# Optimization experiments

Measured on AMD Instinct MI355X. Metric: run time of the kernel, lower is better.

## Reference

```python
import jax, jax.numpy as jnp
import numpy as np

LN_EPS = 1e-5


def _layernorm(x, gamma, beta):
    mu = jnp.mean(x, axis=-1, keepdims=True)
    var = jnp.mean(jnp.square(x - mu), axis=-1, keepdims=True)
    return (x - mu) / jnp.sqrt(var + LN_EPS) * gamma + beta


def setup_inputs() -> dict:
    key = jax.random.key(0)
    ks = jax.random.split(key, 4)
    B, T, H, L = 32, 2048, 512, 2
    scale = 1.0 / np.sqrt(H)  # matches torch GRU uniform(-1/sqrt(H),1/sqrt(H)) scale
    x = jax.random.normal(ks[0], (B, T, H), dtype=jnp.float32)
    W_ih = jax.random.normal(ks[1], (L, 3 * H, H), dtype=jnp.float32) * scale
    W_hh = jax.random.normal(ks[2], (L, 3 * H, H), dtype=jnp.float32) * scale
    b_ih = jnp.zeros((L, 3 * H), dtype=jnp.float32)
    b_hh = jnp.zeros((L, 3 * H), dtype=jnp.float32)
    gamma = jnp.ones((H,), dtype=jnp.float32)
    beta = jnp.zeros((H,), dtype=jnp.float32)
    return {"x": x, "gamma": gamma, "beta": beta,
            "W_ih": W_ih, "W_hh": W_hh, "b_ih": b_ih, "b_hh": b_hh}


def reference(x, gamma, beta, W_ih, W_hh, b_ih, b_hh):
    # LayerNorm then multi-layer GRU (PyTorch gate order: r, z, n).
    B, T, H = x.shape
    L = W_ih.shape[0]
    h = _layernorm(x, gamma, beta)
    for l in range(L):
        # Precompute input projections for all timesteps: [B, T, 3H]
        xp = jnp.einsum('bth,gh->btg', h, W_ih[l]) + b_ih[l]
        Whh_l = W_hh[l]
        bhh_l = b_hh[l]

        def step(h_prev, xp_t):
            hp = h_prev @ Whh_l.T + bhh_l              # [B, 3H]
            xr, xz, xn = jnp.split(xp_t, 3, axis=-1)
            hr, hz, hn = jnp.split(hp, 3, axis=-1)
            r = jax.nn.sigmoid(xr + hr)
            z = jax.nn.sigmoid(xz + hz)
            n = jnp.tanh(xn + r * hn)
            h_new = (1.0 - z) * n + z * h_prev
            return h_new, h_new

        h0 = jnp.zeros((B, H), dtype=x.dtype)
        _, ys = jax.lax.scan(step, h0, jnp.swapaxes(xp, 0, 1))  # [T, B, H]
        h = jnp.swapaxes(ys, 0, 1)
    return h
```

## Files before the change

kernel.cpp:

```cpp
#include <hip/hip_runtime.h>
#include <hip/hip_fp16.h>

typedef float f32x4 __attribute__((ext_vector_type(4)));
typedef float f32x16 __attribute__((ext_vector_type(16)));
typedef _Float16 half8 __attribute__((ext_vector_type(8)));
typedef _Float16 half2t __attribute__((ext_vector_type(2)));
typedef unsigned int u32;
typedef u32 u32x4v __attribute__((ext_vector_type(4)));

#define DEVI static __device__ __forceinline__

constexpr int BATCH = 32;
constexpr int TLEN  = 2048;
constexpr int HDIM  = 512;
constexpr int G3    = 1536;
constexpr u32 POIS  = 0xFFFFFFFFu;
constexpr int NSLOT = 16;

DEVI float fast_sigmoid(float x) { return 1.0f / (1.0f + __expf(-x)); }

DEVI float fast_tanh(float x) {
  const float ax = fabsf(x);
  const float t = __expf(-2.0f * ax);
  const float r = (1.0f - t) / (1.0f + t);
  return copysignf(r, x);
}

DEVI u32 pack2h(float a, float b) {
  return __builtin_bit_cast(u32, __builtin_amdgcn_cvt_pkrtz(a, b));
}

DEVI u32 llc_load32(const u32* p) {
  return __hip_atomic_load(p, __ATOMIC_RELAXED, __HIP_MEMORY_SCOPE_AGENT);
}
DEVI void llc_store32(u32* p, u32 v) {
  __hip_atomic_store(p, v, __ATOMIC_RELAXED, __HIP_MEMORY_SCOPE_AGENT);
}

DEVI u32x4v llc_load128_async(const u32* p) {
  u32x4v r;
  asm volatile("global_load_dwordx4 %0, %1, off sc0 sc1" : "=&v"(r) : "v"(p));
  return r;
}

DEVI int chk4(u32x4v v) {
  return (int)((v[0] == POIS) | (v[1] == POIS) | (v[2] == POIS) | (v[3] == POIS));
}

__global__ void convert_weights(const float* __restrict__ wih, const float* __restrict__ whh,
                                _Float16* __restrict__ wih_h, _Float16* __restrict__ whh_h)
{
  const size_t n = (size_t)2 * G3 * HDIM;
  for (size_t i = (size_t)blockIdx.x * blockDim.x + threadIdx.x; i < n;
       i += (size_t)gridDim.x * blockDim.x) {
    wih_h[i] = (_Float16)wih[i];
    whh_h[i] = (_Float16)whh[i];
  }
}

__global__ __launch_bounds__(256) void ln_kernel(const float* __restrict__ x,
    const float* __restrict__ gamma, const float* __restrict__ beta,
    _Float16* __restrict__ out)
{
  const int row = blockIdx.x;
  const int tid = threadIdx.x;
  const float* xr = x + (size_t)row * HDIM;
  float a = xr[tid], b = xr[tid + 256];
  float s = a + b, ss = a * a + b * b;
#pragma unroll
  for (int m = 1; m < 64; m <<= 1) {
    s  += __shfl_xor(s, m, 64);
    ss += __shfl_xor(ss, m, 64);
  }
  __shared__ float sb[8];
  const int w = tid >> 6;
  if ((tid & 63) == 0) { sb[w] = s; sb[4 + w] = ss; }
  __syncthreads();
  s  = sb[0] + sb[1] + sb[2] + sb[3];
  ss = sb[4] + sb[5] + sb[6] + sb[7];
  const float mu   = s * (1.0f / HDIM);
  const float var  = ss * (1.0f / HDIM) - mu * mu;
  const float rstd = rsqrtf(var + 1e-5f);
  out[(size_t)row * HDIM + tid]       = (_Float16)((a - mu) * rstd * gamma[tid] + beta[tid]);
  out[(size_t)row * HDIM + tid + 256] = (_Float16)((b - mu) * rstd * gamma[tid + 256] + beta[tid + 256]);
}

__global__ __launch_bounds__(256) void gemm_f16(
    const _Float16* __restrict__ A, const _Float16* __restrict__ W,
    const float* __restrict__ bias, _Float16* __restrict__ C,
    int t0, int lgT)
{
  __shared__ _Float16 As[128][40];
  __shared__ _Float16 Bs[128][40];
  const int bm = blockIdx.x;
  const int bn = blockIdx.y;
  const int tid = threadIdx.x;
  const int lane = tid & 63;
  const int wv = tid >> 6;
  const int wm = wv >> 1, wn = wv & 1;
  const int l15 = lane & 15, g4 = lane >> 4;
  const int tmask = (1 << lgT) - 1;

  f32x4 zero4 = {0.f, 0.f, 0.f, 0.f};
  f32x4 acc[4][4];
#pragma unroll
  for (int i = 0; i < 4; ++i) {
#pragma unroll
    for (int j = 0; j < 4; ++j) acc[i][j] = zero4;
  }

  const int srow = tid >> 2;
  const int scol = (tid & 3) * 8;
  size_t arow[2];
#pragma unroll
  for (int r2 = 0; r2 < 2; ++r2) {
    int m = bm * 128 + r2 * 64 + srow;
    int b = m >> lgT, tt = m & tmask;
    arow[r2] = ((size_t)b * TLEN + (size_t)(t0 + tt)) * HDIM;
  }
  const size_t brow0 = (size_t)(bn * 128 + srow) * HDIM;

  for (int kt = 0; kt < HDIM; kt += 32) {
#pragma unroll
    for (int r2 = 0; r2 < 2; ++r2) {
      *(uint4*)&As[r2 * 64 + srow][scol] = *(const uint4*)&A[arow[r2] + kt + scol];
      *(uint4*)&Bs[r2 * 64 + srow][scol] = *(const uint4*)&W[brow0 + (size_t)r2 * 64 * HDIM + kt + scol];
    }
    __syncthreads();
    half8 af[4], bf[4];
#pragma unroll
    for (int i = 0; i < 4; ++i) af[i] = *(const half8*)&As[wm * 64 + i * 16 + l15][g4 * 8];
#pragma unroll
    for (int j = 0; j < 4; ++j) bf[j] = *(const half8*)&Bs[wn * 64 + j * 16 + l15][g4 * 8];
#pragma unroll
    for (int i = 0; i < 4; ++i) {
#pragma unroll
      for (int j = 0; j < 4; ++j)
        acc[i][j] = __builtin_amdgcn_mfma_f32_16x16x32_f16(af[i], bf[j], acc[i][j], 0, 0, 0);
    }
    __syncthreads();
  }
#pragma unroll
  for (int j = 0; j < 4; ++j) {
    const int col = bn * 128 + wn * 64 + j * 16 + l15;
    const float bi = bias[col];
#pragma unroll
    for (int i = 0; i < 4; ++i) {
      const int mrow = bm * 128 + wm * 64 + i * 16 + g4 * 4;
#pragma unroll
      for (int r = 0; r < 4; ++r)
        C[(size_t)(mrow + r) * G3 + col] = (_Float16)(acc[i][j][r] + bi);
    }
  }
}

__global__ void init_sync(u32* __restrict__ h1ring, u32* __restrict__ h2ring,
                          u32* __restrict__ syncw)
{
  const int i = blockIdx.x * 256 + threadIdx.x;
  const u32 v = (i >> 13) == 0 ? 0u : POIS;
  h1ring[i] = v;
  h2ring[i] = v;
  if (i == 0) syncw[0] = 0u;
}

__global__ __launch_bounds__(512, 1) void gru_fused(
    const u32* __restrict__ xp,
    const u32* __restrict__ whh,
    const u32* __restrict__ wih2,
    const float* __restrict__ bhh,
    const float* __restrict__ bih2,
    float* __restrict__ out,
    u32* __restrict__ h1ring,
    u32* __restrict__ h2ring,
    u32* __restrict__ syncw,
    int t0, int t1, int lgT)
{
  const int l2 = blockIdx.x >> 4;
  const int c  = blockIdx.x & 15;
  const int tid = threadIdx.x;
  const int lane = tid & 63;
  const int w = tid >> 6;
  const int l31 = lane & 31;
  const int kh = lane >> 5;

  __shared__ __align__(16) u32 st_l[32 * 260];
  __shared__ __align__(16) u32 h1_l[32 * 260];
  __shared__ float sg_h[96 * 33];
  __shared__ float sg_i[96 * 33];

  half8 bf[32];
  const bool mfma_w = (w < 3) || (l2 && w < 6);
  if (mfma_w) {
    const int gt = (w < 3) ? w : w - 3;
    const int grow = gt * 512 + c * 32 + l31;
    const u32* wsrc = (w < 3) ? (whh + (size_t)l2 * (G3 * 256)) : wih2;
#pragma unroll
    for (int ks = 0; ks < 32; ++ks)
      bf[ks] = *(const half8*)&wsrc[(size_t)grow * 256 + ks * 8 + kh * 4];
  }

  const int dp = tid & 15;
  const int ga = tid >> 4;
  const float* bhh_l = bhh + l2 * G3;
  float biasH[3][2], biasI[3][2];
#pragma unroll
  for (int gt = 0; gt < 3; ++gt) {
    biasH[gt][0] = bhh_l[gt * 512 + c * 32 + 2 * dp];
    biasH[gt][1] = bhh_l[gt * 512 + c * 32 + 2 * dp + 1];
    biasI[gt][0] = l2 ? bih2[gt * 512 + c * 32 + 2 * dp] : 0.0f;
    biasI[gt][1] = l2 ? bih2[gt * 512 + c * 32 + 2 * dp + 1] : 0.0f;
  }

  u32* const ringOwn = l2 ? h2ring : h1ring;

  for (int t = t0; t < t1; ++t) {
    u32 xu[3];
    if (!l2) {
      const size_t row = ((size_t)(ga << lgT) + (size_t)(t - t0)) * 768;
#pragma unroll
      for (int gt = 0; gt < 3; ++gt)
        xu[gt] = xp[row + gt * 256 + c * 16 + dp];
    }

    const u32* rdA = ringOwn + (size_t)(t & 15) * 8192 + (tid << 2);
    const u32* rdB = h1ring + (size_t)((t + 1) & 15) * 8192 + (tid << 2);
    u32x4v a0, a1, a2, a3, b0, b1, b2, b3;
    while (true) {
      a0 = llc_load128_async(rdA);
      a1 = llc_load128_async(rdA + 2048);
      a2 = llc_load128_async(rdA + 4096);
      a3 = llc_load128_async(rdA + 6144);
      if (l2) {
        b0 = llc_load128_async(rdB);
        b1 = llc_load128_async(rdB + 2048);
        b2 = llc_load128_async(rdB + 4096);
        b3 = llc_load128_async(rdB + 6144);
      }
      u32 prog = 0;
      if (!l2) prog = llc_load32(&syncw[0]);
      asm volatile("s_waitcnt vmcnt(0)" ::: "memory");
      __builtin_amdgcn_sched_barrier(0);
      int bad = chk4(a0) | chk4(a1) | chk4(a2) | chk4(a3);
      if (l2) bad |= chk4(b0) | chk4(b1) | chk4(b2) | chk4(b3);
      else    bad |= (int)((int)prog < t - 3);
      if (!__any(bad)) break;
      __builtin_amdgcn_s_sleep(1);
    }
    {
      const int r0 = tid >> 6;
      const int cc = (tid << 2) & 255;
      *(u32x4v*)&st_l[(0  + r0) * 260 + cc] = a0;
      *(u32x4v*)&st_l[(8  + r0) * 260 + cc] = a1;
      *(u32x4v*)&st_l[(16 + r0) * 260 + cc] = a2;
      *(u32x4v*)&st_l[(24 + r0) * 260 + cc] = a3;
      if (l2) {
        *(u32x4v*)&h1_l[(0  + r0) * 260 + cc] = b0;
        *(u32x4v*)&h1_l[(8  + r0) * 260 + cc] = b1;
        *(u32x4v*)&h1_l[(16 + r0) * 260 + cc] = b2;
        *(u32x4v*)&h1_l[(24 + r0) * 260 + cc] = b3;
      }
    }
    __syncthreads();

    const u32 hpp = st_l[ga * 260 + c * 16 + dp];

    if (mfma_w) {
      f32x16 acc;
#pragma unroll
      for (int i = 0; i < 16; ++i) acc[i] = 0.0f;
      const u32* asrc = (w < 3) ? st_l : h1_l;
#pragma unroll
      for (int ks = 0; ks < 32; ++ks) {
        const half8 af = *(const half8*)&asrc[l31 * 260 + ks * 8 + kh * 4];
        acc = __builtin_amdgcn_mfma_f32_32x32x16_f16(af, bf[ks], acc, 0, 0, 0);
      }
      const int gt = (w < 3) ? w : w - 3;
      float* sg = (w < 3) ? sg_h : sg_i;
#pragma unroll
      for (int r = 0; r < 16; ++r) {
        const int grp = (r & 3) + 8 * (r >> 2) + 4 * kh;
        sg[(gt * 32 + l31) * 33 + grp] = acc[r];
      }
    }
    __syncthreads();

    float hn0, hn1;
    {
      const half2t hp2 = __builtin_bit_cast(half2t, hpp);
      float hn[2];
#pragma unroll
      for (int dd = 0; dd < 2; ++dd) {
        const int d = 2 * dp + dd;
        float xr, xz, xn;
        if (!l2) {
          const half2t xr2 = __builtin_bit_cast(half2t, xu[0]);
          const half2t xz2 = __builtin_bit_cast(half2t, xu[1]);
          const half2t xn2 = __builtin_bit_cast(half2t, xu[2]);
          xr = (float)(dd ? xr2.y : xr2.x);
          xz = (float)(dd ? xz2.y : xz2.x);
          xn = (float)(dd ? xn2.y : xn2.x);
        } else {
          xr = sg_i[(0 * 32 + d) * 33 + ga] + biasI[0][dd];
          xz = sg_i[(32 + d) * 33 + ga]     + biasI[1][dd];
          xn = sg_i[(64 + d) * 33 + ga]     + biasI[2][dd];
        }
        const float hprev = (float)(dd ? hp2.y : hp2.x);
        const float rr = fast_sigmoid(xr + sg_h[(0 * 32 + d) * 33 + ga] + biasH[0][dd]);
        const float zz = fast_sigmoid(xz + sg_h[(32 + d) * 33 + ga]     + biasH[1][dd]);
        const float nn = fast_tanh(xn + rr * (sg_h[(64 + d) * 33 + ga]  + biasH[2][dd]));
        hn[dd] = (1.0f - zz) * nn + zz * hprev;
      }
      hn0 = hn[0]; hn1 = hn[1];
    }
    const int my = ga * 256 + c * 16 + dp;
    llc_store32(&ringOwn[(size_t)((t + 1) & 15) * 8192 + my], pack2h(hn0, hn1));
    if (l2) {
      float2 v; v.x = hn0; v.y = hn1;
      *(float2*)&out[((size_t)ga * TLEN + t) * HDIM + c * 32 + 2 * dp] = v;
    }
    llc_store32(&ringOwn[(size_t)((t + 9) & 15) * 8192 + my], POIS);
    if (l2 && c == 0 && tid == 0) llc_store32(&syncw[0], (u32)(t + 1));
  }
}

extern "C" void kernel_launch(void* const* d_in, const int* in_sizes, int n_in,
                              void* d_out, int out_size, void* d_ws, size_t ws_size,
                              hipStream_t stream)
{
  const float* x     = (const float*)d_in[0];
  const float* gamma = (const float*)d_in[1];
  const float* beta  = (const float*)d_in[2];
  const float* Wih   = (const float*)d_in[3];
  const float* Whh   = (const float*)d_in[4];
  const float* bih   = (const float*)d_in[5];
  const float* bhh   = (const float*)d_in[6];
  float* out = (float*)d_out;

  const size_t wbytes  = (size_t)2 * G3 * HDIM * 2;
  const size_t hseqb   = (size_t)BATCH * TLEN * HDIM * 2;
  const size_t ringb   = (size_t)NSLOT * 8192 * 4;
  const size_t fixed   = hseqb + 2 * wbytes + 2 * ringb + 4096;
  int lgT = 11;
  while (lgT > 2 && ((size_t)BATCH * ((size_t)1 << lgT) * G3 * 2 + fixed) > ws_size) --lgT;
  const int TSEG = 1 << lgT;
  const int nseg = TLEN / TSEG;

  char* ws = (char*)d_ws;
  _Float16* xp     = (_Float16*)ws;
  char* base       = ws + (size_t)BATCH * TSEG * G3 * 2;
  _Float16* hseq   = (_Float16*)base;
  _Float16* wih_h  = (_Float16*)(base + hseqb);
  _Float16* whh_h  = (_Float16*)(base + hseqb + wbytes);
  u32*      h1ring = (u32*)    (base + hseqb + 2 * wbytes);
  u32*      h2ring = h1ring + (size_t)NSLOT * 8192;
  u32*      syncw  = h2ring + (size_t)NSLOT * 8192;

  convert_weights<<<512, 256, 0, stream>>>(Wih, Whh, wih_h, whh_h);
  ln_kernel<<<BATCH * TLEN, 256, 0, stream>>>(x, gamma, beta, hseq);
  init_sync<<<512, 256, 0, stream>>>(h1ring, h2ring, syncw);

  const dim3 ggrid(BATCH * TSEG / 128, 12);
  for (int s = 0; s < nseg; ++s) {
    const int t0 = s * TSEG;
    gemm_f16<<<ggrid, 256, 0, stream>>>(hseq, wih_h, bih, xp, t0, lgT);
    gru_fused<<<32, 512, 0, stream>>>((const u32*)xp, (const u32*)whh_h,
                                      (const u32*)(wih_h + (size_t)G3 * HDIM),
                                      bhh, bih + G3, out,
                                      h1ring, h2ring, syncw, t0, t0 + TSEG, lgT);
  }
}
```

Measured before the change: 8.701 ms.

## Restructure GRU recurrence MFMA into 16x16 tiles with in-register gate epilogue

The recurrent matmul moves from three 32x32x16 MFMA waves to four waves of 16x16x32 MFMA. Each wave computes all three gates for its own 16x16 tile, so the gate nonlinearity runs straight from accumulators and the sg_h LDS round trip and one barrier in layer 1 go away. The ring buffer layout changes to a per-block chunked fp16 layout written with 16-bit atomic stores, and the poison check now works per half. Each block's own previous h slice is read from LDS instead of polled from the ring. In exchange each writing thread issues more, smaller global stores, and a barrier is added at the end of every step.

```diff
diff --git a/kernel.cpp b/kernel.cpp
--- a/kernel.cpp
+++ b/kernel.cpp
@@ -6,6 +6,7 @@
 typedef _Float16 half8 __attribute__((ext_vector_type(8)));
 typedef _Float16 half2t __attribute__((ext_vector_type(2)));
 typedef unsigned int u32;
+typedef unsigned short u16;
 typedef u32 u32x4v __attribute__((ext_vector_type(4)));
 
 #define DEVI static __device__ __forceinline__
@@ -36,6 +37,9 @@
 DEVI void llc_store32(u32* p, u32 v) {
   __hip_atomic_store(p, v, __ATOMIC_RELAXED, __HIP_MEMORY_SCOPE_AGENT);
 }
+DEVI void llc_store16(u16* p, u16 v) {
+  __hip_atomic_store(p, v, __ATOMIC_RELAXED, __HIP_MEMORY_SCOPE_AGENT);
+}
 
 DEVI u32x4v llc_load128_async(const u32* p) {
   u32x4v r;
@@ -43,8 +47,14 @@
   return r;
 }
 
-DEVI int chk4(u32x4v v) {
-  return (int)((v[0] == POIS) | (v[1] == POIS) | (v[2] == POIS) | (v[3] == POIS));
+DEVI int chkH(u32x4v v) {
+  int b = 0;
+#pragma unroll
+  for (int i = 0; i < 4; ++i) {
+    const u32 x = v[i];
+    b |= (int)(((x & 0xFFFFu) == 0xFFFFu) | ((x >> 16) == 0xFFFFu));
+  }
+  return b;
 }
 
 __global__ void convert_weights(const float* __restrict__ wih, const float* __restrict__ whh,
@@ -181,48 +191,76 @@
   const int tid = threadIdx.x;
   const int lane = tid & 63;
   const int w = tid >> 6;
-  const int l31 = lane & 31;
-  const int kh = lane >> 5;
+  const int l15 = lane & 15;
+  const int g4 = (lane >> 4) & 3;
 
   __shared__ __align__(16) u32 st_l[32 * 260];
   __shared__ __align__(16) u32 h1_l[32 * 260];
-  __shared__ float sg_h[96 * 33];
   __shared__ float sg_i[96 * 33];
-
-  half8 bf[32];
-  const bool mfma_w = (w < 3) || (l2 && w < 6);
-  if (mfma_w) {
-    const int gt = (w < 3) ? w : w - 3;
+  __shared__ __align__(16) _Float16 own_h[1024];
+  u32* const own_hU = (u32*)own_h;
+
+  const bool isHH = (w < 4);
+  const bool isIH = l2 && (w >= 4) && (w < 7);
+  const int dh = w & 1, gh = (w >> 1) & 1;
+  const int db = dh * 16 + l15;
+
+  const u32* whL = whh + (size_t)l2 * (G3 * 256);
+  half8 bfh[3][16];
+  if (isHH) {
+#pragma unroll
+    for (int gt = 0; gt < 3; ++gt) {
+      const int grow = gt * 512 + c * 32 + db;
+#pragma unroll
+      for (int ks = 0; ks < 16; ++ks) {
+        union { uint4 q; half8 h; } u;
+        u.q = *(const uint4*)&whL[(size_t)grow * 256 + ks * 16 + g4 * 4];
+        bfh[gt][ks] = u.h;
+      }
+    }
+  }
+  half8 bfi[32];
+  if (isIH) {
+    const int gt = w - 4, l31 = lane & 31, kh2 = lane >> 5;
     const int grow = gt * 512 + c * 32 + l31;
-    const u32* wsrc = (w < 3) ? (whh + (size_t)l2 * (G3 * 256)) : wih2;
-#pragma unroll
-    for (int ks = 0; ks < 32; ++ks)
-      bf[ks] = *(const half8*)&wsrc[(size_t)grow * 256 + ks * 8 + kh * 4];
-  }
-
-  const int dp = tid & 15;
-  const int ga = tid >> 4;
-  const float* bhh_l = bhh + l2 * G3;
-  float biasH[3][2], biasI[3][2];
-#pragma unroll
-  for (int gt = 0; gt < 3; ++gt) {
-    biasH[gt][0] = bhh_l[gt * 512 + c * 32 + 2 * dp];
-    biasH[gt][1] = bhh_l[gt * 512 + c * 32 + 2 * dp + 1];
-    biasI[gt][0] = l2 ? bih2[gt * 512 + c * 32 + 2 * dp] : 0.0f;
-    biasI[gt][1] = l2 ? bih2[gt * 512 + c * 32 + 2 * dp + 1] : 0.0f;
-  }
+#pragma unroll
+    for (int ks = 0; ks < 32; ++ks) {
+      union { uint4 q; half8 h; } u;
+      u.q = *(const uint4*)&wih2[(size_t)grow * 256 + ks * 8 + kh2 * 4];
+      bfi[ks] = u.h;
+    }
+  }
+  float bH[3] = {0, 0, 0}, bI[3] = {0, 0, 0};
+  if (isHH) {
+#pragma unroll
+    for (int gt = 0; gt < 3; ++gt) {
+      bH[gt] = bhh[l2 * G3 + gt * 512 + c * 32 + db];
+      bI[gt] = l2 ? bih2[gt * 512 + c * 32 + db] : 0.0f;
+    }
+  }
+
+  const int dp0 = (tid & 3) << 2;
+  const int gaS = (tid >> 2) & 31;
+  const int cs0 = tid >> 7;
+  const int jOwn = (cs0 == (c & 3)) ? (c >> 2) : -1;
 
   u32* const ringOwn = l2 ? h2ring : h1ring;
+  u16* const ringOwnH = (u16*)ringOwn;
 
   for (int t = t0; t < t1; ++t) {
-    u32 xu[3];
-    if (!l2) {
-      const size_t row = ((size_t)(ga << lgT) + (size_t)(t - t0)) * 768;
-#pragma unroll
-      for (int gt = 0; gt < 3; ++gt)
-        xu[gt] = xp[row + gt * 256 + c * 16 + dp];
-    }
-
+    u32 xu[3][4];
+    if (!l2 && isHH) {
+      const int tl = t - t0;
+#pragma unroll
+      for (int r = 0; r < 4; ++r) {
+        const int g = gh * 16 + g4 * 4 + r;
+        const size_t rowp = ((size_t)(g << lgT) + (size_t)tl) * 768;
+#pragma unroll
+        for (int gt = 0; gt < 3; ++gt)
+          xu[gt][r] = xp[rowp + gt * 256 + c * 16 + (db >> 1)];
+      }
+    }
+    const int jSkip = (t != t0) ? jOwn : -1;
     const u32* rdA = ringOwn + (size_t)(t & 15) * 8192 + (tid << 2);
     const u32* rdB = h1ring + (size_t)((t + 1) & 15) * 8192 + (tid << 2);
     u32x4v a0, a1, a2, a3, b0, b1, b2, b3;
@@ -241,86 +279,95 @@
       if (!l2) prog = llc_load32(&syncw[0]);
       asm volatile("s_waitcnt vmcnt(0)" ::: "memory");
       __builtin_amdgcn_sched_barrier(0);
-      int bad = chk4(a0) | chk4(a1) | chk4(a2) | chk4(a3);
-      if (l2) bad |= chk4(b0) | chk4(b1) | chk4(b2) | chk4(b3);
+      int bad = 0;
+      if (jSkip != 0) bad |= chkH(a0);
+      if (jSkip != 1) bad |= chkH(a1);
+      if (jSkip != 2) bad |= chkH(a2);
+      if (jSkip != 3) bad |= chkH(a3);
+      if (l2) bad |= chkH(b0) | chkH(b1) | chkH(b2) | chkH(b3);
       else    bad |= (int)((int)prog < t - 3);
       if (!__any(bad)) break;
       __builtin_amdgcn_s_sleep(1);
     }
-    {
-      const int r0 = tid >> 6;
-      const int cc = (tid << 2) & 255;
-      *(u32x4v*)&st_l[(0  + r0) * 260 + cc] = a0;
-      *(u32x4v*)&st_l[(8  + r0) * 260 + cc] = a1;
-      *(u32x4v*)&st_l[(16 + r0) * 260 + cc] = a2;
-      *(u32x4v*)&st_l[(24 + r0) * 260 + cc] = a3;
-      if (l2) {
-        *(u32x4v*)&h1_l[(0  + r0) * 260 + cc] = b0;
-        *(u32x4v*)&h1_l[(8  + r0) * 260 + cc] = b1;
-        *(u32x4v*)&h1_l[(16 + r0) * 260 + cc] = b2;
-        *(u32x4v*)&h1_l[(24 + r0) * 260 + cc] = b3;
-      }
+    if (jSkip == 0) a0 = *(const u32x4v*)&own_hU[gaS * 16 + dp0];
+    if (jSkip == 1) a1 = *(const u32x4v*)&own_hU[gaS * 16 + dp0];
+    if (jSkip == 2) a2 = *(const u32x4v*)&own_hU[gaS * 16 + dp0];
+    if (jSkip == 3) a3 = *(const u32x4v*)&own_hU[gaS * 16 + dp0];
+    *(u32x4v*)&st_l[gaS * 260 + (cs0 + 0)  * 16 + dp0] = a0;
+    *(u32x4v*)&st_l[gaS * 260 + (cs0 + 4)  * 16 + dp0] = a1;
+    *(u32x4v*)&st_l[gaS * 260 + (cs0 + 8)  * 16 + dp0] = a2;
+    *(u32x4v*)&st_l[gaS * 260 + (cs0 + 12) * 16 + dp0] = a3;
+    if (l2) {
+      *(u32x4v*)&h1_l[gaS * 260 + (cs0 + 0)  * 16 + dp0] = b0;
+      *(u32x4v*)&h1_l[gaS * 260 + (cs0 + 4)  * 16 + dp0] = b1;
+      *(u32x4v*)&h1_l[gaS * 260 + (cs0 + 8)  * 16 + dp0] = b2;
+      *(u32x4v*)&h1_l[gaS * 260 + (cs0 + 12) * 16 + dp0] = b3;
     }
     __syncthreads();
 
-    const u32 hpp = st_l[ga * 260 + c * 16 + dp];
-
-    if (mfma_w) {
-      f32x16 acc;
-#pragma unroll
-      for (int i = 0; i < 16; ++i) acc[i] = 0.0f;
-      const u32* asrc = (w < 3) ? st_l : h1_l;
-#pragma unroll
-      for (int ks = 0; ks < 32; ++ks) {
-        const half8 af = *(const half8*)&asrc[l31 * 260 + ks * 8 + kh * 4];
-        acc = __builtin_amdgcn_mfma_f32_32x32x16_f16(af, bf[ks], acc, 0, 0, 0);
-      }
-      const int gt = (w < 3) ? w : w - 3;
-      float* sg = (w < 3) ? sg_h : sg_i;
-#pragma unroll
-      for (int r = 0; r < 16; ++r) {
-        const int grp = (r & 3) + 8 * (r >> 2) + 4 * kh;
-        sg[(gt * 32 + l31) * 33 + grp] = acc[r];
-      }
-    }
-    __syncthreads();
-
-    float hn0, hn1;
-    {
-      const half2t hp2 = __builtin_bit_cast(half2t, hpp);
-      float hn[2];
-#pragma unroll
-      for (int dd = 0; dd < 2; ++dd) {
-        const int d = 2 * dp + dd;
+    f32x4 ah0 = {0, 0, 0, 0}, ah1 = {0, 0, 0, 0}, ah2 = {0, 0, 0, 0};
+    if (isHH) {
+#pragma unroll
+      for (int ks = 0; ks < 16; ++ks) {
+        const half8 af = *(const half8*)&st_l[(gh * 16 + l15) * 260 + ks * 16 + g4 * 4];
+        ah0 = __builtin_amdgcn_mfma_f32_16x16x32_f16(af, bfh[0][ks], ah0, 0, 0, 0);
+        ah1 = __builtin_amdgcn_mfma_f32_16x16x32_f16(af, bfh[1][ks], ah1, 0, 0, 0);
+        ah2 = __builtin_amdgcn_mfma_f32_16x16x32_f16(af, bfh[2][ks], ah2, 0, 0, 0);
+      }
+    }
+    if (l2) {
+      if (isIH) {
+        const int gt = w - 4, l31 = lane & 31, kh2 = lane >> 5;
+        f32x16 acc;
+#pragma unroll
+        for (int i = 0; i < 16; ++i) acc[i] = 0.0f;
+#pragma unroll
+        for (int ks = 0; ks < 32; ++ks) {
+          const half8 af = *(const half8*)&h1_l[l31 * 260 + ks * 8 + kh2 * 4];
+          acc = __builtin_amdgcn_mfma_f32_32x32x16_f16(af, bfi[ks], acc, 0, 0, 0);
+        }
+#pragma unroll
+        for (int r = 0; r < 16; ++r) {
+          const int grp = (r & 3) + 8 * (r >> 2) + 4 * kh2;
+          sg_i[(gt * 32 + l31) * 33 + grp] = acc[r];
+        }
+      }
+      __syncthreads();
+    }
+
+    if (isHH) {
+#pragma unroll
+      for (int r = 0; r < 4; ++r) {
+        const int g = gh * 16 + g4 * 4 + r;
+        const half2t hp2 = __builtin_bit_cast(half2t, st_l[g * 260 + c * 16 + (db >> 1)]);
+        const float hprev = (float)((db & 1) ? hp2.y : hp2.x);
         float xr, xz, xn;
         if (!l2) {
-          const half2t xr2 = __builtin_bit_cast(half2t, xu[0]);
-          const half2t xz2 = __builtin_bit_cast(half2t, xu[1]);
-          const half2t xn2 = __builtin_bit_cast(half2t, xu[2]);
-          xr = (float)(dd ? xr2.y : xr2.x);
-          xz = (float)(dd ? xz2.y : xz2.x);
-          xn = (float)(dd ? xn2.y : xn2.x);
+          const half2t x0 = __builtin_bit_cast(half2t, xu[0][r]);
+          const half2t x1 = __builtin_bit_cast(half2t, xu[1][r]);
+          const half2t x2 = __builtin_bit_cast(half2t, xu[2][r]);
+          xr = (float)((db & 1) ? x0.y : x0.x);
+          xz = (float)((db & 1) ? x1.y : x1.x);
+          xn = (float)((db & 1) ? x2.y : x2.x);
         } else {
-          xr = sg_i[(0 * 32 + d) * 33 + ga] + biasI[0][dd];
-          xz = sg_i[(32 + d) * 33 + ga]     + biasI[1][dd];
-          xn = sg_i[(64 + d) * 33 + ga]     + biasI[2][dd];
+          xr = sg_i[(0  + db) * 33 + g] + bI[0];
+          xz = sg_i[(32 + db) * 33 + g] + bI[1];
+          xn = sg_i[(64 + db) * 33 + g] + bI[2];
         }
-        const float hprev = (float)(dd ? hp2.y : hp2.x);
-        const float rr = fast_sigmoid(xr + sg_h[(0 * 32 + d) * 33 + ga] + biasH[0][dd]);
-        const float zz = fast_sigmoid(xz + sg_h[(32 + d) * 33 + ga]     + biasH[1][dd]);
-        const float nn = fast_tanh(xn + rr * (sg_h[(64 + d) * 33 + ga]  + biasH[2][dd]));
-        hn[dd] = (1.0f - zz) * nn + zz * hprev;
-      }
-      hn0 = hn[0]; hn1 = hn[1];
-    }
-    const int my = ga * 256 + c * 16 + dp;
-    llc_store32(&ringOwn[(size_t)((t + 1) & 15) * 8192 + my], pack2h(hn0, hn1));
-    if (l2) {
-      float2 v; v.x = hn0; v.y = hn1;
-      *(float2*)&out[((size_t)ga * TLEN + t) * HDIM + c * 32 + 2 * dp] = v;
-    }
-    llc_store32(&ringOwn[(size_t)((t + 9) & 15) * 8192 + my], POIS);
+        const float rr = fast_sigmoid(xr + ah0[r] + bH[0]);
+        const float zz = fast_sigmoid(xz + ah1[r] + bH[1]);
+        const float nn = fast_tanh(xn + rr * (ah2[r] + bH[2]));
+        const float hn = (1.0f - zz) * nn + zz * hprev;
+        const _Float16 hf = (_Float16)hn;
+        llc_store16(&ringOwnH[(size_t)((t + 1) & 15) * 16384 + c * 1024 + g * 32 + db],
+                    __builtin_bit_cast(u16, hf));
+        own_h[g * 32 + db] = hf;
+        if (l2) out[((size_t)g * TLEN + t) * HDIM + c * 32 + db] = hn;
+      }
+    }
+    llc_store32(&ringOwn[(size_t)((t + 9) & 15) * 8192 + c * 512 + tid], POIS);
     if (l2 && c == 0 && tid == 0) llc_store32(&syncw[0], (u32)(t + 1));
+    __syncthreads();
   }
 }
 
```

After: 22.02 ms. +153.1%, slower.
